# Kernel optimization log

Hardware: AMD Instinct MI355X
Metric: run time of the kernel (lower is better)

## Reference

```python
import jax, jax.numpy as jnp
import numpy as np


def setup_inputs() -> dict:
    key = jax.random.key(0)
    k1, k2 = jax.random.split(key)
    n, c, H, W = 8, 16, 512, 512
    pred = jax.random.normal(k1, (n, c, H, W), dtype=jnp.float32)
    target = jax.random.randint(k2, (n, H, W), 0, c, dtype=jnp.int64)
    weights = jnp.ones((n, 1, H, W), dtype=jnp.float32)  # ignored by the module
    return {"pred": pred, "target": target, "weights": weights}


def reference(pred, target, weights):
    # pred: [n,c,H,W] logits; target: [n,H,W] int class ids; weights arg is ignored
    n, c, H, W = pred.shape
    # Global (whole-batch) per-class pixel counts -> inverse-frequency weights.
    counts = jnp.zeros((c,), dtype=pred.dtype).at[target.reshape(-1)].add(1.0)
    w_class = jnp.where(counts > 0, 1.0 / (counts * c), 0.0)  # [c]
    w = w_class[target]  # [n,H,W] per-pixel weight (constant w.r.t. pred)
    # log-softmax gathered at target class per pixel
    logp = jax.nn.log_softmax(pred, axis=1)  # [n,c,H,W]
    lp_t = jnp.take_along_axis(logp, target[:, None, :, :], axis=1)[:, 0]  # [n,H,W]
    num = (lp_t * w).reshape(n, -1).sum(axis=1)  # [n]
    den = w.reshape(n, -1).sum(axis=1)           # [n]
    return -(num / den).mean()
```

## Files before the change

kernel.cpp:

```cpp
#include <hip/hip_runtime.h>

#define NIMG 8
#define NCLS 16
#define HW   262144
#define NBIN (NIMG * NCLS)

__global__ __launch_bounds__(256) void dwce_main(const float* __restrict__ pred,
                                                 const int* __restrict__ tgt,
                                                 float* __restrict__ ws) {
    __shared__ float s_sum[NBIN];
    __shared__ float s_cnt[NBIN];
    const int tid = threadIdx.x;
    if (tid < NBIN) { s_sum[tid] = 0.0f; s_cnt[tid] = 0.0f; }
    __syncthreads();

    const long long thread_id = (long long)blockIdx.x * blockDim.x + tid;
    const long long p0 = thread_id * 4;
    const int n_img = (int)(p0 >> 18);
    const int hw    = (int)(p0 & (HW - 1));
    const float* base = pred + ((size_t)n_img * NCLS) * HW + hw;

    float4 v[NCLS];
#pragma unroll
    for (int c = 0; c < NCLS; ++c)
        v[c] = *(const float4*)(base + (size_t)c * HW);

    int4 t = *(const int4*)(tgt + p0);

    float4 m = v[0];
#pragma unroll
    for (int c = 1; c < NCLS; ++c) {
        m.x = fmaxf(m.x, v[c].x);
        m.y = fmaxf(m.y, v[c].y);
        m.z = fmaxf(m.z, v[c].z);
        m.w = fmaxf(m.w, v[c].w);
    }
    float4 s = make_float4(0.f, 0.f, 0.f, 0.f);
    float xt0 = 0.f, xt1 = 0.f, xt2 = 0.f, xt3 = 0.f;
#pragma unroll
    for (int c = 0; c < NCLS; ++c) {
        s.x += __expf(v[c].x - m.x);
        s.y += __expf(v[c].y - m.y);
        s.z += __expf(v[c].z - m.z);
        s.w += __expf(v[c].w - m.w);
        if (t.x == c) xt0 = v[c].x;
        if (t.y == c) xt1 = v[c].y;
        if (t.z == c) xt2 = v[c].z;
        if (t.w == c) xt3 = v[c].w;
    }
    const float lp0 = xt0 - (m.x + __logf(s.x));
    const float lp1 = xt1 - (m.y + __logf(s.y));
    const float lp2 = xt2 - (m.z + __logf(s.z));
    const float lp3 = xt3 - (m.w + __logf(s.w));

    const int b = n_img * NCLS;
    atomicAdd(&s_sum[b + t.x], lp0);
    atomicAdd(&s_sum[b + t.y], lp1);
    atomicAdd(&s_sum[b + t.z], lp2);
    atomicAdd(&s_sum[b + t.w], lp3);
    atomicAdd(&s_cnt[b + t.x], 1.0f);
    atomicAdd(&s_cnt[b + t.y], 1.0f);
    atomicAdd(&s_cnt[b + t.z], 1.0f);
    atomicAdd(&s_cnt[b + t.w], 1.0f);

    __syncthreads();
    if (tid < NBIN) {
        unsafeAtomicAdd(&ws[tid],        s_sum[tid]);
        unsafeAtomicAdd(&ws[NBIN + tid], s_cnt[tid]);
    }
}

__global__ __launch_bounds__(128) void dwce_final(const float* __restrict__ ws,
                                                  float* __restrict__ out) {
    __shared__ float sum[NBIN];
    __shared__ float cnt[NBIN];
    __shared__ float wcl[NCLS];
    __shared__ float ratio[NIMG];
    const int tid = threadIdx.x;
    sum[tid] = ws[tid];
    cnt[tid] = ws[NBIN + tid];
    __syncthreads();
    if (tid < NCLS) {
        float g = 0.f;
#pragma unroll
        for (int i = 0; i < NIMG; ++i) g += cnt[i * NCLS + tid];
        wcl[tid] = (g > 0.f) ? 1.0f / (g * (float)NCLS) : 0.0f;
    }
    __syncthreads();
    if (tid < NIMG) {
        float num = 0.f, den = 0.f;
#pragma unroll
        for (int c = 0; c < NCLS; ++c) {
            num += sum[tid * NCLS + c] * wcl[c];
            den += cnt[tid * NCLS + c] * wcl[c];
        }
        ratio[tid] = num / den;
    }
    __syncthreads();
    if (tid == 0) {
        float r = 0.f;
#pragma unroll
        for (int i = 0; i < NIMG; ++i) r += ratio[i];
        out[0] = -r * (1.0f / (float)NIMG);
    }
}

extern "C" void kernel_launch(void* const* d_in, const int* in_sizes, int n_in,
                              void* d_out, int out_size, void* d_ws, size_t ws_size,
                              hipStream_t stream) {
    const float* pred = (const float*)d_in[0];
    const int*   tgt  = (const int*)d_in[1];
    float* out = (float*)d_out;
    float* ws  = (float*)d_ws;

    hipMemsetAsync(ws, 0, 2 * NBIN * sizeof(float), stream);

    const int total_threads = (NIMG * HW) / 4;
    dwce_main<<<total_threads / 256, 256, 0, stream>>>(pred, tgt, ws);
    dwce_final<<<1, 128, 0, stream>>>(ws, out);
}
```

Measured before the change: 220.4 us.

## Use online softmax with double-buffered loads and per-block partials instead of atomics

The main kernel now loads the 16 class planes in chunks of four with double buffering and an online max/sum rescale, which reduces live registers. Each block covers a single image, so shared bins shrink to 32 entries. Blocks write their partial sums to a strided partials array rather than doing global atomics, and this removes the memset launch. The final kernel reduces the 2048 partials per bin with vectorized loads. The cost is extra exp work from the rescaling and a heavier final reduction.

Result: faster. 208.8 us (-5.3%).

```diff
diff --git a/kernel.cpp b/kernel.cpp
--- a/kernel.cpp
+++ b/kernel.cpp
@@ -3,96 +3,125 @@
 #define NIMG 8
 #define NCLS 16
 #define HW   262144
-#define NBIN (NIMG * NCLS)
+#define NBLK 2048
 
 __global__ __launch_bounds__(256) void dwce_main(const float* __restrict__ pred,
                                                  const int* __restrict__ tgt,
-                                                 float* __restrict__ ws) {
-    __shared__ float s_sum[NBIN];
-    __shared__ float s_cnt[NBIN];
+                                                 float* __restrict__ partials) {
+    __shared__ float s_bin[32];
     const int tid = threadIdx.x;
-    if (tid < NBIN) { s_sum[tid] = 0.0f; s_cnt[tid] = 0.0f; }
+    if (tid < 32) s_bin[tid] = 0.0f;
     __syncthreads();
 
-    const long long thread_id = (long long)blockIdx.x * blockDim.x + tid;
-    const long long p0 = thread_id * 4;
+    const int gid = blockIdx.x * 256 + tid;
+    const long long p0 = (long long)gid * 4;
     const int n_img = (int)(p0 >> 18);
     const int hw    = (int)(p0 & (HW - 1));
-    const float* base = pred + ((size_t)n_img * NCLS) * HW + hw;
+    const float* base = pred + (size_t)n_img * NCLS * HW + hw;
 
-    float4 v[NCLS];
+    const int4 t = *(const int4*)(tgt + p0);
+
+    float4 v[2][4];
 #pragma unroll
-    for (int c = 0; c < NCLS; ++c)
-        v[c] = *(const float4*)(base + (size_t)c * HW);
+    for (int j = 0; j < 4; ++j)
+        v[0][j] = *(const float4*)(base + (size_t)j * HW);
 
-    int4 t = *(const int4*)(tgt + p0);
+    float4 m  = make_float4(-3.0e38f, -3.0e38f, -3.0e38f, -3.0e38f);
+    float4 s  = make_float4(0.f, 0.f, 0.f, 0.f);
+    float4 xt = make_float4(0.f, 0.f, 0.f, 0.f);
 
-    float4 m = v[0];
 #pragma unroll
-    for (int c = 1; c < NCLS; ++c) {
-        m.x = fmaxf(m.x, v[c].x);
-        m.y = fmaxf(m.y, v[c].y);
-        m.z = fmaxf(m.z, v[c].z);
-        m.w = fmaxf(m.w, v[c].w);
+    for (int chunk = 0; chunk < 4; ++chunk) {
+        const int cur = chunk & 1;
+        if (chunk < 3) {
+#pragma unroll
+            for (int j = 0; j < 4; ++j)
+                v[cur ^ 1][j] = *(const float4*)(base + (size_t)((chunk + 1) * 4 + j) * HW);
+        }
+        float4 mc = v[cur][0];
+#pragma unroll
+        for (int j = 1; j < 4; ++j) {
+            mc.x = fmaxf(mc.x, v[cur][j].x);
+            mc.y = fmaxf(mc.y, v[cur][j].y);
+            mc.z = fmaxf(mc.z, v[cur][j].z);
+            mc.w = fmaxf(mc.w, v[cur][j].w);
+        }
+        float4 mn;
+        mn.x = fmaxf(m.x, mc.x);
+        mn.y = fmaxf(m.y, mc.y);
+        mn.z = fmaxf(m.z, mc.z);
+        mn.w = fmaxf(m.w, mc.w);
+        s.x *= __expf(m.x - mn.x);
+        s.y *= __expf(m.y - mn.y);
+        s.z *= __expf(m.z - mn.z);
+        s.w *= __expf(m.w - mn.w);
+#pragma unroll
+        for (int j = 0; j < 4; ++j) {
+            const int c = chunk * 4 + j;
+            const float4 vv = v[cur][j];
+            s.x += __expf(vv.x - mn.x);
+            s.y += __expf(vv.y - mn.y);
+            s.z += __expf(vv.z - mn.z);
+            s.w += __expf(vv.w - mn.w);
+            if (t.x == c) xt.x = vv.x;
+            if (t.y == c) xt.y = vv.y;
+            if (t.z == c) xt.z = vv.z;
+            if (t.w == c) xt.w = vv.w;
+        }
+        m = mn;
     }
-    float4 s = make_float4(0.f, 0.f, 0.f, 0.f);
-    float xt0 = 0.f, xt1 = 0.f, xt2 = 0.f, xt3 = 0.f;
-#pragma unroll
-    for (int c = 0; c < NCLS; ++c) {
-        s.x += __expf(v[c].x - m.x);
-        s.y += __expf(v[c].y - m.y);
-        s.z += __expf(v[c].z - m.z);
-        s.w += __expf(v[c].w - m.w);
-        if (t.x == c) xt0 = v[c].x;
-        if (t.y == c) xt1 = v[c].y;
-        if (t.z == c) xt2 = v[c].z;
-        if (t.w == c) xt3 = v[c].w;
-    }
-    const float lp0 = xt0 - (m.x + __logf(s.x));
-    const float lp1 = xt1 - (m.y + __logf(s.y));
-    const float lp2 = xt2 - (m.z + __logf(s.z));
-    const float lp3 = xt3 - (m.w + __logf(s.w));
 
-    const int b = n_img * NCLS;
-    atomicAdd(&s_sum[b + t.x], lp0);
-    atomicAdd(&s_sum[b + t.y], lp1);
-    atomicAdd(&s_sum[b + t.z], lp2);
-    atomicAdd(&s_sum[b + t.w], lp3);
-    atomicAdd(&s_cnt[b + t.x], 1.0f);
-    atomicAdd(&s_cnt[b + t.y], 1.0f);
-    atomicAdd(&s_cnt[b + t.z], 1.0f);
-    atomicAdd(&s_cnt[b + t.w], 1.0f);
+    const float lp0 = xt.x - (m.x + __logf(s.x));
+    const float lp1 = xt.y - (m.y + __logf(s.y));
+    const float lp2 = xt.z - (m.z + __logf(s.z));
+    const float lp3 = xt.w - (m.w + __logf(s.w));
+
+    atomicAdd(&s_bin[t.x], lp0);
+    atomicAdd(&s_bin[t.y], lp1);
+    atomicAdd(&s_bin[t.z], lp2);
+    atomicAdd(&s_bin[t.w], lp3);
+    atomicAdd(&s_bin[16 + t.x], 1.0f);
+    atomicAdd(&s_bin[16 + t.y], 1.0f);
+    atomicAdd(&s_bin[16 + t.z], 1.0f);
+    atomicAdd(&s_bin[16 + t.w], 1.0f);
 
     __syncthreads();
-    if (tid < NBIN) {
-        unsafeAtomicAdd(&ws[tid],        s_sum[tid]);
-        unsafeAtomicAdd(&ws[NBIN + tid], s_cnt[tid]);
-    }
+    if (tid < 32)
+        partials[(size_t)tid * NBLK + blockIdx.x] = s_bin[tid];
 }
 
-__global__ __launch_bounds__(128) void dwce_final(const float* __restrict__ ws,
+__global__ __launch_bounds__(256) void dwce_final(const float* __restrict__ ws,
                                                   float* __restrict__ out) {
-    __shared__ float sum[NBIN];
-    __shared__ float cnt[NBIN];
+    __shared__ float tot[32][NIMG];
     __shared__ float wcl[NCLS];
     __shared__ float ratio[NIMG];
     const int tid = threadIdx.x;
-    sum[tid] = ws[tid];
-    cnt[tid] = ws[NBIN + tid];
+    const int c = tid >> 3;
+    const int n = tid & 7;
+
+    const float4* p = (const float4*)(ws + (size_t)c * NBLK + n * 256);
+    float4 a = make_float4(0.f, 0.f, 0.f, 0.f);
+#pragma unroll 8
+    for (int k = 0; k < 64; ++k) {
+        float4 q = p[k];
+        a.x += q.x; a.y += q.y; a.z += q.z; a.w += q.w;
+    }
+    tot[c][n] = (a.x + a.y) + (a.z + a.w);
     __syncthreads();
+
     if (tid < NCLS) {
         float g = 0.f;
 #pragma unroll
-        for (int i = 0; i < NIMG; ++i) g += cnt[i * NCLS + tid];
+        for (int i = 0; i < NIMG; ++i) g += tot[NCLS + tid][i];
         wcl[tid] = (g > 0.f) ? 1.0f / (g * (float)NCLS) : 0.0f;
     }
     __syncthreads();
     if (tid < NIMG) {
         float num = 0.f, den = 0.f;
 #pragma unroll
-        for (int c = 0; c < NCLS; ++c) {
-            num += sum[tid * NCLS + c] * wcl[c];
-            den += cnt[tid * NCLS + c] * wcl[c];
+        for (int c2 = 0; c2 < NCLS; ++c2) {
+            num += tot[c2][tid] * wcl[c2];
+            den += tot[NCLS + c2][tid] * wcl[c2];
         }
         ratio[tid] = num / den;
     }
@@ -113,9 +142,6 @@
     float* out = (float*)d_out;
     float* ws  = (float*)d_ws;
 
-    hipMemsetAsync(ws, 0, 2 * NBIN * sizeof(float), stream);
-
-    const int total_threads = (NIMG * HW) / 4;
-    dwce_main<<<total_threads / 256, 256, 0, stream>>>(pred, tgt, ws);
-    dwce_final<<<1, 128, 0, stream>>>(ws, out);
+    dwce_main<<<NBLK, 256, 0, stream>>>(pred, tgt, ws);
+    dwce_final<<<1, 256, 0, stream>>>(ws, out);
 }
```
